# Kernel optimization log

Hardware: AMD Instinct MI355X
Metric: run time of the kernel (lower is better)

The kernel has to match this reference:

```python
import jax, jax.numpy as jnp
import numpy as np

B, T, C = 4, 4096, 256

def setup_inputs() -> dict:
    key = jax.random.key(0)
    ks = jax.random.split(key, 7)
    s = 1.0 / np.sqrt(C)
    return {
        "x": jax.random.normal(ks[0], (B, T, C), dtype=jnp.float32),
        "Wq": jax.random.uniform(ks[1], (C, C), jnp.float32, -s, s),
        "bq": jax.random.uniform(ks[2], (C,), jnp.float32, -s, s),
        "Wk": jax.random.uniform(ks[3], (C, C), jnp.float32, -s, s),
        "bk": jax.random.uniform(ks[4], (C,), jnp.float32, -s, s),
        "Wv": jax.random.uniform(ks[5], (C, C), jnp.float32, -s, s),
        "bv": jax.random.uniform(ks[6], (C,), jnp.float32, -s, s),
    }

def reference(x, Wq, bq, Wk, bk, Wv, bv):
    # Projections (torch Linear: y = x @ W^T + b; here W stored as [in,out])
    q = x @ Wq + bq  # [B,T,C]
    k = x @ Wk + bk
    v = x @ Wv + bv
    dk = q.shape[-1]
    scores = jnp.einsum('btc,bsc->bts', q, k) / jnp.sqrt(jnp.float32(dk))
    Tn = x.shape[1]
    causal = jnp.tril(jnp.ones((Tn, Tn), dtype=bool))  # [T,T]
    scores = jnp.where(causal[None, :, :], scores, jnp.float32(-1e9))
    attn = jax.nn.softmax(scores, axis=-1)
    return jnp.einsum('bts,bsc->btc', attn, v)
```

## Files before the change

kernel.cpp:

```cpp
#include <hip/hip_runtime.h>
#include <hip/hip_bf16.h>

#define T_SEQ 4096
#define DIM   256
#define NBATCH 4

typedef short s8v __attribute__((ext_vector_type(8)));
typedef float f4v __attribute__((ext_vector_type(4)));
typedef unsigned short u16;

#define MFMA16(a,b,c) __builtin_amdgcn_mfma_f32_16x16x32_bf16(a,b,c,0,0,0)
#define FENCE_LGKM() asm volatile("s_waitcnt lgkmcnt(0)" ::: "memory")

__device__ int g_cnt[4];

static __device__ __forceinline__ u16 f2bf(float f) {
  union { float f; unsigned int u; } c; c.f = f;
  unsigned int u = c.u;
  unsigned int r = (u + 0x7fffu + ((u >> 16) & 1u)) >> 16;
  return (u16)r;
}

static __device__ __forceinline__ s8v pack8(const float* p) {
  float4 a = *(const float4*)p;
  float4 b = *(const float4*)(p + 4);
  s8v r;
  r[0] = (short)f2bf(a.x); r[1] = (short)f2bf(a.y);
  r[2] = (short)f2bf(a.z); r[3] = (short)f2bf(a.w);
  r[4] = (short)f2bf(b.x); r[5] = (short)f2bf(b.y);
  r[6] = (short)f2bf(b.z); r[7] = (short)f2bf(b.w);
  return r;
}

static __device__ __forceinline__ void gll16(const u16* g, u16* l) {
  __builtin_amdgcn_global_load_lds(
      (const __attribute__((address_space(1))) unsigned int*)g,
      (__attribute__((address_space(3))) unsigned int*)l, 16, 0, 0);
}

__global__ void diag_fill_kernel(float* __restrict__ out, float val, int n) {
  int i = blockIdx.x * blockDim.x + threadIdx.x;
  if (i < n) out[i] = val;
}

__global__ void wtrans_kernel(const float* __restrict__ Wq, const float* __restrict__ Wk,
                              const float* __restrict__ Wv, u16* __restrict__ Wt) {
  if (blockIdx.x == 0 && blockIdx.y == 0 && blockIdx.z == 0 &&
      threadIdx.y == 0 && threadIdx.x < 4)
    g_cnt[threadIdx.x] = 0;
  __shared__ float tile[32][33];
  int m = blockIdx.z;
  const float* W = (m == 0) ? Wq : ((m == 1) ? Wk : Wv);
  int bx = blockIdx.x * 32, by = blockIdx.y * 32;
  int x = threadIdx.x, y = threadIdx.y;
  #pragma unroll
  for (int i = 0; i < 32; i += 8) tile[y + i][x] = W[(by + y + i) * DIM + bx + x];
  __syncthreads();
  u16* o = Wt + m * DIM * DIM;
  #pragma unroll
  for (int i = 0; i < 32; i += 8) o[(bx + y + i) * DIM + by + x] = f2bf(tile[x][y + i]);
}

__global__ __launch_bounds__(256) void proj_kernel(
    const float* __restrict__ x, const u16* __restrict__ Wt,
    const float* __restrict__ bq, const float* __restrict__ bk, const float* __restrict__ bv,
    u16* __restrict__ qf, u16* __restrict__ kf, u16* __restrict__ vf) {
  alignas(16) __shared__ u16 Kl[64 * 264];
  alignas(16) __shared__ u16 Vl[256 * 72];

  int bid = blockIdx.x;
  int which = blockIdx.y;
  int tid  = threadIdx.x;
  int wave = tid >> 6, lane = tid & 63, quad = lane >> 4, l16 = lane & 15;
  int row0 = bid * 64 + wave * 16;

  s8v a[8];
  const float* xp = x + (size_t)(row0 + l16) * DIM + quad * 8;
  #pragma unroll
  for (int ks = 0; ks < 8; ks++) a[ks] = pack8(xp + ks * 32);

  if (which == 0) {
    const u16* W = Wt + DIM * DIM;
    f4v acc[16];
    #pragma unroll
    for (int nt = 0; nt < 16; nt++) acc[nt] = (f4v){0.f, 0.f, 0.f, 0.f};
    #pragma unroll
    for (int ks = 0; ks < 8; ks++) {
      #pragma unroll
      for (int nt = 0; nt < 16; nt++) {
        s8v bfr = *(const s8v*)(W + (nt * 16 + l16) * DIM + ks * 32 + quad * 8);
        acc[nt] = MFMA16(a[ks], bfr, acc[nt]);
      }
    }
    #pragma unroll
    for (int nt = 0; nt < 16; nt++) {
      float bb = bk[nt * 16 + l16];
      #pragma unroll
      for (int r = 0; r < 4; r++)
        Kl[(wave * 16 + quad * 4 + r) * 264 + nt * 16 + l16] = f2bf(acc[nt][r] + bb);
    }
    __syncthreads();
    #pragma unroll
    for (int i = 0; i < 8; i++) {
      int o = tid + i * 256;
      int tile = o >> 10, rem = o & 1023;
      int f = rem >> 6, ln = rem & 63;
      int sl = tile * 32 + (f >> 3) * 16 + (ln & 15);
      int c  = (f & 7) * 32 + (ln >> 4) * 8;
      s8v v = *(const s8v*)&Kl[sl * 264 + c];
      *(s8v*)&kf[(((size_t)(bid * 2 + tile) * 16 + f) * 64 + ln) * 8] = v;
    }
  } else if (which == 1) {
    const u16* W = Wt + 2 * DIM * DIM;
    f4v acc[16];
    #pragma unroll
    for (int nt = 0; nt < 16; nt++) acc[nt] = (f4v){0.f, 0.f, 0.f, 0.f};
    #pragma unroll
    for (int ks = 0; ks < 8; ks++) {
      #pragma unroll
      for (int nt = 0; nt < 16; nt++) {
        s8v bfr = *(const s8v*)(W + (nt * 16 + l16) * DIM + ks * 32 + quad * 8);
        acc[nt] = MFMA16(a[ks], bfr, acc[nt]);
      }
    }
    #pragma unroll
    for (int nt = 0; nt < 16; nt++) {
      float bb = bv[nt * 16 + l16];
      union { u16 h[4]; uint2 v2; } pk;
      #pragma unroll
      for (int r = 0; r < 4; r++) pk.h[r] = f2bf(acc[nt][r] + bb);
      *(uint2*)&Vl[(nt * 16 + l16) * 72 + wave * 16 + quad * 4] = pk.v2;
    }
    __syncthreads();
    #pragma unroll
    for (int i = 0; i < 8; i++) {
      int o = tid + i * 256;
      int tile = o >> 10, rem = o & 1023;
      int nt = rem >> 6, ln = rem & 63;
      int c  = nt * 16 + (ln & 15);
      int sl = tile * 32 + (ln >> 4) * 8;
      s8v v = *(const s8v*)&Vl[c * 72 + sl];
      *(s8v*)&vf[(((size_t)(bid * 2 + tile) * 16 + nt) * 64 + ln) * 8] = v;
    }
  } else {
    const u16* W = Wt;
    f4v acc[16];
    #pragma unroll
    for (int nt = 0; nt < 16; nt++) acc[nt] = (f4v){0.f, 0.f, 0.f, 0.f};
    #pragma unroll
    for (int ks = 0; ks < 8; ks++) {
      #pragma unroll
      for (int nt = 0; nt < 16; nt++) {
        s8v bfr = *(const s8v*)(W + (nt * 16 + l16) * DIM + ks * 32 + quad * 8);
        acc[nt] = MFMA16(a[ks], bfr, acc[nt]);
      }
    }
    #pragma unroll
    for (int nt = 0; nt < 16; nt++) {
      float bb = bq[nt * 16 + l16];
      #pragma unroll
      for (int r = 0; r < 4; r++)
        Kl[(wave * 16 + quad * 4 + r) * 264 + nt * 16 + l16] =
            f2bf((acc[nt][r] + bb) * 0.0625f);
    }
    __syncthreads();
    #pragma unroll
    for (int i = 0; i < 8; i++) {
      int o = tid + i * 256;
      int tile = o >> 10, rem = o & 1023;
      int f = rem >> 6, ln = rem & 63;
      int sl = tile * 32 + (f >> 3) * 16 + (ln & 15);
      int c  = (f & 7) * 32 + (ln >> 4) * 8;
      s8v v = *(const s8v*)&Kl[sl * 264 + c];
      *(s8v*)&qf[(((size_t)(bid * 2 + tile) * 16 + f) * 64 + ln) * 8] = v;
    }
  }
}

__global__ __launch_bounds__(1024, 4) void attn_kernel(
    const u16* __restrict__ qf, const u16* __restrict__ kf, const u16* __restrict__ vf,
    float* __restrict__ Opart, float* __restrict__ lpart, float* __restrict__ out) {
  alignas(16) __shared__ u16 KVa[16384];
  alignas(16) __shared__ u16 KVb[16384];
  alignas(16) __shared__ u16 Ps[8 * 640];
  __shared__ float lbuf[8][2][16];
  __shared__ int taskS;

  int bid = blockIdx.x, b = bid & 3;
  int tid = threadIdx.x;
  int w = tid >> 6, lane = tid & 63, quad = lane >> 4, l16 = lane & 15;
  int s = w >> 1, h = w & 1;

  const u16* qfb = qf + (size_t)b * 128 * 8192;
  const u16* kfb = kf + (size_t)b * 128 * 8192;
  const u16* vfb = vf + (size_t)b * 128 * 8192;

  for (;;) {
    if (tid == 0) taskS = atomicAdd(&g_cnt[b], 1);
    __syncthreads();
    int t = taskS;
    if (t >= 80) break;
    int q, c;
    if (t < 8)        { q = 24 + t;        c = 0; }
    else if (t < 16)  { q = 24 + (t - 8);  c = 1; }
    else if (t < 24)  { q = 24 + (t - 16); c = 2; }
    else if (t == 24) { q = 31;            c = 3; }
    else if (t < 33)  { q = 16 + (t - 25); c = 0; }
    else if (t < 41)  { q = 16 + (t - 33); c = 1; }
    else if (t == 41) { q = 23;            c = 2; }
    else if (t < 50)  { q = 8 + (t - 42);  c = 0; }
    else if (t == 50) { q = 15;            c = 1; }
    else if (t == 51) { q = 7;             c = 0; }
    else { int u = t - 52, sz = u >> 2, band = u & 3;
           if (band == 0)      { q = 6 - sz;  c = 0; }
           else if (band == 1) { q = 14 - sz; c = 1; }
           else if (band == 2) { q = 22 - sz; c = 2; }
           else                { q = 30 - sz; c = 3; } }
    int row0 = q * 128;
    int n = 4 * q + 4;
    int lo = c * 32, hi = min(n, lo + 32);
    int nch = (q + 8) >> 3;

    s8v qa[8];
    {
      const u16* qt = qfb + (((size_t)(q * 4 + (s >> 1)) * 16 + (s & 1) * 8) * 64) * 8;
      #pragma unroll
      for (int ks = 0; ks < 8; ks++) qa[ks] = *(const s8v*)(qt + (ks * 64 + lane) * 8);
    }

    {
      const u16* kt = kfb + ((size_t)lo << 13);
      const u16* vt = vfb + ((size_t)lo << 13);
      gll16(kt + (w << 9) + (lane << 3), &KVa[w << 9]);
      gll16(vt + (w << 9) + (lane << 3), &KVa[8192 + (w << 9)]);
    }
    __syncthreads();

    int rowBase = row0 + (s << 4);
    f4v o[8];
    #pragma unroll
    for (int nt = 0; nt < 8; nt++) o[nt] = (f4v){0.f, 0.f, 0.f, 0.f};
    float lrow[4] = {0.f, 0.f, 0.f, 0.f};

    auto iter_body = [&](const u16* buf, int kvi) {
      f4v cc = (f4v){0.f, 0.f, 0.f, 0.f};
      #pragma unroll
      for (int ks = 0; ks < 8; ks++) {
        s8v kfr = *(const s8v*)&buf[(((h << 3) + ks) << 9) + (lane << 3)];
        cc = MFMA16(qa[ks], kfr, cc);
      }
      int s0 = kvi * 32 + (h << 4) + l16;
      #pragma unroll
      for (int r = 0; r < 4; r++) {
        int tq = rowBase + (quad << 2) + r;
        float p = __expf((s0 > tq) ? -1e30f : cc[r]);
        Ps[s * 640 + ((quad << 2) + r) * 40 + (h << 4) + l16] = f2bf(p);
        lrow[r] += p;
      }
      FENCE_LGKM();
      __builtin_amdgcn_sched_barrier(0);
      __builtin_amdgcn_s_barrier();
      __builtin_amdgcn_sched_barrier(0);
      s8v pa = *(const s8v*)&Ps[s * 640 + l16 * 40 + (quad << 3)];
      #pragma unroll
      for (int nt = 0; nt < 8; nt++) {
        s8v vfr = *(const s8v*)&buf[8192 + (((h << 3) + nt) << 9) + (lane << 3)];
        o[nt] = MFMA16(pa, vfr, o[nt]);
      }
    };

    #pragma unroll 1
    for (int kv = lo; kv < hi; kv += 2) {
      {
        const u16* kt = kfb + ((size_t)(kv + 1) << 13);
        const u16* vt = vfb + ((size_t)(kv + 1) << 13);
        gll16(kt + (w << 9) + (lane << 3), &KVb[w << 9]);
        gll16(vt + (w << 9) + (lane << 3), &KVb[8192 + (w << 9)]);
      }
      iter_body(KVa, kv);
      __syncthreads();
      if (kv + 2 < hi) {
        const u16* kt = kfb + ((size_t)(kv + 2) << 13);
        const u16* vt = vfb + ((size_t)(kv + 2) << 13);
        gll16(kt + (w << 9) + (lane << 3), &KVa[w << 9]);
        gll16(vt + (w << 9) + (lane << 3), &KVa[8192 + (w << 9)]);
      }
      iter_body(KVb, kv + 1);
      __syncthreads();
    }

    #pragma unroll
    for (int r = 0; r < 4; r++) {
      #pragma unroll
      for (int d = 1; d < 16; d <<= 1) lrow[r] += __shfl_xor(lrow[r], d);
    }
    if (l16 == 0) {
      #pragma unroll
      for (int r = 0; r < 4; r++) lbuf[s][h][(quad << 2) + r] = lrow[r];
    }
    __syncthreads();

    if (nch == 1) {
      #pragma unroll
      for (int nt = 0; nt < 8; nt++) {
        #pragma unroll
        for (int r = 0; r < 4; r++) {
          float ls = lbuf[s][0][(quad << 2) + r] + lbuf[s][1][(quad << 2) + r];
          out[(size_t)(b * T_SEQ + rowBase + (quad << 2) + r) * DIM +
              ((h * 8 + nt) * 16 + l16)] = o[nt][r] / ls;
        }
      }
    } else {
      int slotB = (q < 16) ? (q - 8) * 2
                : (q < 24) ? 16 + (q - 16) * 3
                           : 40 + (q - 24) * 4;
      int slot = b * 72 + slotB + c;
      float* Op = Opart + ((size_t)slot << 15);
      #pragma unroll
      for (int nt = 0; nt < 8; nt++) {
        #pragma unroll
        for (int r = 0; r < 4; r++)
          Op[((s << 4) + (quad << 2) + r) * 256 + (h * 8 + nt) * 16 + l16] = o[nt][r];
      }
      if (h == 0 && l16 == 0) {
        #pragma unroll
        for (int r = 0; r < 4; r++)
          lpart[slot * 128 + (s << 4) + (quad << 2) + r] =
              lbuf[s][0][(quad << 2) + r] + lbuf[s][1][(quad << 2) + r];
      }
    }
  }
}

__global__ void combine_kernel(const float* __restrict__ Opart,
                               const float* __restrict__ lpart,
                               float* __restrict__ out) {
  int blk = blockIdx.x;
  int b = blk & 3;
  int rest = blk >> 2;
  int q = 8 + (rest >> 3);
  int g = rest & 7;
  int col = threadIdx.x;
  int nch = (q + 8) >> 3;
  int slotB = (q < 16) ? (q - 8) * 2
            : (q < 24) ? 16 + (q - 16) * 3
                       : 40 + (q - 24) * 4;
  int slot0 = b * 72 + slotB;
  #pragma unroll 4
  for (int i = 0; i < 16; i++) {
    int rt = g * 16 + i;
    float acc = 0.f, ls = 0.f;
    for (int c = 0; c < nch; c++) {
      acc += Opart[(((size_t)(slot0 + c)) << 15) + rt * 256 + col];
      ls  += lpart[(slot0 + c) * 128 + rt];
    }
    out[(size_t)(b * T_SEQ + q * 128 + rt) * DIM + col] = acc / ls;
  }
}

extern "C" void kernel_launch(void* const* d_in, const int* in_sizes, int n_in,
                              void* d_out, int out_size, void* d_ws, size_t ws_size,
                              hipStream_t stream) {
  const float* x  = (const float*)d_in[0];
  const float* Wq = (const float*)d_in[1];
  const float* bq = (const float*)d_in[2];
  const float* Wk = (const float*)d_in[3];
  const float* bk = (const float*)d_in[4];
  const float* Wv = (const float*)d_in[5];
  const float* bv = (const float*)d_in[6];

  const size_t NTD = (size_t)NBATCH * T_SEQ * DIM;
  const size_t WT_ELEMS = (size_t)3 * DIM * DIM;
  const size_t NSLOT = 288;
  const size_t REQ_BYTES = (WT_ELEMS + 3 * NTD) * sizeof(u16)
                         + NSLOT * 32768 * sizeof(float)
                         + NSLOT * 128 * sizeof(float);

  if (ws_size < REQ_BYTES) {
    float val = (float)(ws_size >> 20);
    diag_fill_kernel<<<(out_size + 255) / 256, 256, 0, stream>>>((float*)d_out, val, out_size);
    return;
  }

  u16* ws = (u16*)d_ws;
  u16* WT = ws;
  u16* Kf = ws + WT_ELEMS;
  u16* Vf = Kf + NTD;
  u16* Qf = Vf + NTD;
  float* Opart = (float*)(Qf + NTD);
  float* lpart = Opart + NSLOT * 32768;

  wtrans_kernel<<<dim3(8, 8, 3), dim3(32, 8, 1), 0, stream>>>(Wq, Wk, Wv, WT);
  proj_kernel<<<dim3(256, 3, 1), dim3(256, 1, 1), 0, stream>>>(x, WT, bq, bk, bv, Qf, Kf, Vf);
  attn_kernel<<<dim3(256, 1, 1), dim3(1024, 1, 1), 0, stream>>>(Qf, Kf, Vf,
                                                                Opart, lpart, (float*)d_out);
  combine_kernel<<<dim3(768, 1, 1), dim3(256, 1, 1), 0, stream>>>(Opart, lpart, (float*)d_out);
}
```

Before: 212.2 us.

## Halve attention query tile to 64 rows with 512-thread blocks and retuned schedule

Shrinks each attention task from a 128-row to a 64-row query tile. Blocks drop from 16 waves to 8 and the grid doubles to 512 blocks, with 160 tasks per batch and 4 KV chunks per task. Each wave now issues two K and two V async loads per stage. The partial-output slot layout and the combine kernel are resized to match. The goal is finer-grained load balancing across the causal triangle and less per-block barrier contention, at the cost of streaming each K/V tile from L2 twice as often per output row.

```diff
diff --git a/kernel.cpp b/kernel.cpp
--- a/kernel.cpp
+++ b/kernel.cpp
@@ -177,13 +177,13 @@
   }
 }
 
-__global__ __launch_bounds__(1024, 4) void attn_kernel(
+__global__ __launch_bounds__(512, 4) void attn_kernel(
     const u16* __restrict__ qf, const u16* __restrict__ kf, const u16* __restrict__ vf,
     float* __restrict__ Opart, float* __restrict__ lpart, float* __restrict__ out) {
   alignas(16) __shared__ u16 KVa[16384];
   alignas(16) __shared__ u16 KVb[16384];
-  alignas(16) __shared__ u16 Ps[8 * 640];
-  __shared__ float lbuf[8][2][16];
+  alignas(16) __shared__ u16 Ps[4 * 640];
+  __shared__ float lbuf[4][2][16];
   __shared__ int taskS;
 
   int bid = blockIdx.x, b = bid & 3;
@@ -199,31 +199,28 @@
     if (tid == 0) taskS = atomicAdd(&g_cnt[b], 1);
     __syncthreads();
     int t = taskS;
-    if (t >= 80) break;
+    if (t >= 160) break;
     int q, c;
-    if (t < 8)        { q = 24 + t;        c = 0; }
-    else if (t < 16)  { q = 24 + (t - 8);  c = 1; }
-    else if (t < 24)  { q = 24 + (t - 16); c = 2; }
-    else if (t == 24) { q = 31;            c = 3; }
-    else if (t < 33)  { q = 16 + (t - 25); c = 0; }
-    else if (t < 41)  { q = 16 + (t - 33); c = 1; }
-    else if (t == 41) { q = 23;            c = 2; }
-    else if (t < 50)  { q = 8 + (t - 42);  c = 0; }
-    else if (t == 50) { q = 15;            c = 1; }
-    else if (t == 51) { q = 7;             c = 0; }
-    else { int u = t - 52, sz = u >> 2, band = u & 3;
-           if (band == 0)      { q = 6 - sz;  c = 0; }
-           else if (band == 1) { q = 14 - sz; c = 1; }
-           else if (band == 2) { q = 22 - sz; c = 2; }
-           else                { q = 30 - sz; c = 3; } }
-    int row0 = q * 128;
-    int n = 4 * q + 4;
+    if (t < 48)       { q = 48 + (t & 15); c = t >> 4; }
+    else if (t < 80)  { q = 32 + ((t - 48) & 15); c = (t - 48) >> 4; }
+    else if (t < 96)  { q = 16 + (t - 80); c = 0; }
+    else if (t == 96) { q = 15; c = 0; }
+    else if (t == 97) { q = 31; c = 1; }
+    else if (t == 98) { q = 47; c = 2; }
+    else if (t == 99) { q = 63; c = 3; }
+    else { int u = t - 100, sz = u >> 2, band = u & 3;
+           if (band == 0)      { q = 14 - sz; c = 0; }
+           else if (band == 1) { q = 30 - sz; c = 1; }
+           else if (band == 2) { q = 46 - sz; c = 2; }
+           else                { q = 62 - sz; c = 3; } }
+    int row0 = q * 64;
+    int n = 2 * q + 2;
     int lo = c * 32, hi = min(n, lo + 32);
-    int nch = (q + 8) >> 3;
+    int nch = (q >> 4) + 1;
 
     s8v qa[8];
     {
-      const u16* qt = qfb + (((size_t)(q * 4 + (s >> 1)) * 16 + (s & 1) * 8) * 64) * 8;
+      const u16* qt = qfb + (((size_t)(q * 2 + (s >> 1)) * 16 + (s & 1) * 8) * 64) * 8;
       #pragma unroll
       for (int ks = 0; ks < 8; ks++) qa[ks] = *(const s8v*)(qt + (ks * 64 + lane) * 8);
     }
@@ -231,8 +228,12 @@
     {
       const u16* kt = kfb + ((size_t)lo << 13);
       const u16* vt = vfb + ((size_t)lo << 13);
-      gll16(kt + (w << 9) + (lane << 3), &KVa[w << 9]);
-      gll16(vt + (w << 9) + (lane << 3), &KVa[8192 + (w << 9)]);
+      #pragma unroll
+      for (int i = 0; i < 2; i++) {
+        int ch = (w << 1) + i;
+        gll16(kt + (ch << 9) + (lane << 3), &KVa[ch << 9]);
+        gll16(vt + (ch << 9) + (lane << 3), &KVa[8192 + (ch << 9)]);
+      }
     }
     __syncthreads();
 
@@ -274,16 +275,24 @@
       {
         const u16* kt = kfb + ((size_t)(kv + 1) << 13);
         const u16* vt = vfb + ((size_t)(kv + 1) << 13);
-        gll16(kt + (w << 9) + (lane << 3), &KVb[w << 9]);
-        gll16(vt + (w << 9) + (lane << 3), &KVb[8192 + (w << 9)]);
+        #pragma unroll
+        for (int i = 0; i < 2; i++) {
+          int ch = (w << 1) + i;
+          gll16(kt + (ch << 9) + (lane << 3), &KVb[ch << 9]);
+          gll16(vt + (ch << 9) + (lane << 3), &KVb[8192 + (ch << 9)]);
+        }
       }
       iter_body(KVa, kv);
       __syncthreads();
       if (kv + 2 < hi) {
         const u16* kt = kfb + ((size_t)(kv + 2) << 13);
         const u16* vt = vfb + ((size_t)(kv + 2) << 13);
-        gll16(kt + (w << 9) + (lane << 3), &KVa[w << 9]);
-        gll16(vt + (w << 9) + (lane << 3), &KVa[8192 + (w << 9)]);
+        #pragma unroll
+        for (int i = 0; i < 2; i++) {
+          int ch = (w << 1) + i;
+          gll16(kt + (ch << 9) + (lane << 3), &KVa[ch << 9]);
+          gll16(vt + (ch << 9) + (lane << 3), &KVa[8192 + (ch << 9)]);
+        }
       }
       iter_body(KVb, kv + 1);
       __syncthreads();
@@ -311,11 +320,11 @@
         }
       }
     } else {
-      int slotB = (q < 16) ? (q - 8) * 2
-                : (q < 24) ? 16 + (q - 16) * 3
-                           : 40 + (q - 24) * 4;
-      int slot = b * 72 + slotB + c;
-      float* Op = Opart + ((size_t)slot << 15);
+      int slotB = (q < 32) ? (q - 16) * 2
+                : (q < 48) ? 32 + (q - 32) * 3
+                           : 80 + (q - 48) * 4;
+      int slot = b * 144 + slotB + c;
+      float* Op = Opart + ((size_t)slot << 14);
       #pragma unroll
       for (int nt = 0; nt < 8; nt++) {
         #pragma unroll
@@ -325,7 +334,7 @@
       if (h == 0 && l16 == 0) {
         #pragma unroll
         for (int r = 0; r < 4; r++)
-          lpart[slot * 128 + (s << 4) + (quad << 2) + r] =
+          lpart[slot * 64 + (s << 4) + (quad << 2) + r] =
               lbuf[s][0][(quad << 2) + r] + lbuf[s][1][(quad << 2) + r];
       }
     }
@@ -338,23 +347,23 @@
   int blk = blockIdx.x;
   int b = blk & 3;
   int rest = blk >> 2;
-  int q = 8 + (rest >> 3);
-  int g = rest & 7;
+  int q = 16 + (rest >> 2);
+  int g = rest & 3;
   int col = threadIdx.x;
-  int nch = (q + 8) >> 3;
-  int slotB = (q < 16) ? (q - 8) * 2
-            : (q < 24) ? 16 + (q - 16) * 3
-                       : 40 + (q - 24) * 4;
-  int slot0 = b * 72 + slotB;
+  int nch = (q >> 4) + 1;
+  int slotB = (q < 32) ? (q - 16) * 2
+            : (q < 48) ? 32 + (q - 32) * 3
+                       : 80 + (q - 48) * 4;
+  int slot0 = b * 144 + slotB;
   #pragma unroll 4
   for (int i = 0; i < 16; i++) {
     int rt = g * 16 + i;
     float acc = 0.f, ls = 0.f;
     for (int c = 0; c < nch; c++) {
-      acc += Opart[(((size_t)(slot0 + c)) << 15) + rt * 256 + col];
-      ls  += lpart[(slot0 + c) * 128 + rt];
-    }
-    out[(size_t)(b * T_SEQ + q * 128 + rt) * DIM + col] = acc / ls;
+      acc += Opart[(((size_t)(slot0 + c)) << 14) + rt * 256 + col];
+      ls  += lpart[(slot0 + c) * 64 + rt];
+    }
+    out[(size_t)(b * T_SEQ + q * 64 + rt) * DIM + col] = acc / ls;
   }
 }
 
@@ -371,10 +380,10 @@
 
   const size_t NTD = (size_t)NBATCH * T_SEQ * DIM;
   const size_t WT_ELEMS = (size_t)3 * DIM * DIM;
-  const size_t NSLOT = 288;
+  const size_t NSLOT = 576;
   const size_t REQ_BYTES = (WT_ELEMS + 3 * NTD) * sizeof(u16)
-                         + NSLOT * 32768 * sizeof(float)
-                         + NSLOT * 128 * sizeof(float);
+                         + NSLOT * 16384 * sizeof(float)
+                         + NSLOT * 64 * sizeof(float);
 
   if (ws_size < REQ_BYTES) {
     float val = (float)(ws_size >> 20);
@@ -388,11 +397,11 @@
   u16* Vf = Kf + NTD;
   u16* Qf = Vf + NTD;
   float* Opart = (float*)(Qf + NTD);
-  float* lpart = Opart + NSLOT * 32768;
+  float* lpart = Opart + NSLOT * 16384;
 
   wtrans_kernel<<<dim3(8, 8, 3), dim3(32, 8, 1), 0, stream>>>(Wq, Wk, Wv, WT);
   proj_kernel<<<dim3(256, 3, 1), dim3(256, 1, 1), 0, stream>>>(x, WT, bq, bk, bv, Qf, Kf, Vf);
-  attn_kernel<<<dim3(256, 1, 1), dim3(1024, 1, 1), 0, stream>>>(Qf, Kf, Vf,
-                                                                Opart, lpart, (float*)d_out);
+  attn_kernel<<<dim3(512, 1, 1), dim3(512, 1, 1), 0, stream>>>(Qf, Kf, Vf,
+                                                               Opart, lpart, (float*)d_out);
   combine_kernel<<<dim3(768, 1, 1), dim3(256, 1, 1), 0, stream>>>(Opart, lpart, (float*)d_out);
 }
```

New measurement: 218.0 us. +2.7%, slower.
